# Kernel optimization log

Measured on AMD Instinct MI355X. Metric: run time of the kernel, lower is better.

The kernel has to match this reference:

```python
import jax, jax.numpy as jnp
import numpy as np

C0, C1 = 8, 4            # scalar / vector channels (type_in = type_out = [8,4])
K = 5                    # p-space kernel size
G = 8                    # number of gaussian radial basis functions
EPS = 1e-6               # zero-length epsilon
R_MAX = 5.5              # max |p_off - q_diff| ~ sqrt(3)*2 + 2


def _levi_civita():
    e = np.zeros((3, 3, 3), np.float32)
    e[0, 1, 2] = e[1, 2, 0] = e[2, 0, 1] = 1.0
    e[0, 2, 1] = e[2, 1, 0] = e[1, 0, 2] = -1.0
    return jnp.asarray(e)


def setup_inputs() -> dict:
    key = jax.random.key(0)
    ks = jax.random.split(key, 10)
    N, Q, P = 1, 16, 8
    dim = C0 + 3 * C1
    x = jax.random.normal(ks[0], (N, dim, Q, P, P, P), jnp.float32)

    def qschema(k):
        q = jax.random.normal(k, (Q, 3), jnp.float32)
        return q / jnp.max(jnp.linalg.norm(q, axis=-1))  # normalize lengths to <= 1

    q_in, q_out = qschema(ks[1]), qschema(ks[2])
    s = 0.1
    w_ss = s * jax.random.normal(ks[3], (C0, C0, G), jnp.float32)
    w_vs = s * jax.random.normal(ks[4], (C1, C0, G), jnp.float32)
    w_sv = s * jax.random.normal(ks[5], (C0, C1, G), jnp.float32)
    w_vv0 = s * jax.random.normal(ks[6], (C1, C1, G), jnp.float32)
    w_vv1 = s * jax.random.normal(ks[7], (C1, C1, G), jnp.float32)
    bias = s * jax.random.normal(ks[8], (C0,), jnp.float32)
    return dict(x=x, q_in=q_in, q_out=q_out, w_ss=w_ss, w_vs=w_vs, w_sv=w_sv,
                w_vv0=w_vv0, w_vv1=w_vv1, bias=bias)


def reference(x, q_in, q_out, w_ss, w_vs, w_sv, w_vv0, w_vv1, bias):
    N, dim_in, Qi = x.shape[0], x.shape[1], x.shape[2]
    Qo = q_out.shape[0]
    K3 = K ** 3
    # p-space tap offsets (voxel units, zyx) of the 5x5x5 kernel
    offs = jnp.arange(K, dtype=x.dtype) - (K - 1) / 2.0
    oz, oy, ox = jnp.meshgrid(offs, offs, offs, indexing='ij')
    p_off = jnp.stack([oz, oy, ox], -1).reshape(-1, 3)                       # (K3,3)
    # pq_diff geometry: v = p_offset - (q_out - q_in)
    v = p_off[None, None] - (q_out[:, None, None] - q_in[None, :, None])     # (Qo,Qi,K3,3)
    r = jnp.linalg.norm(v, axis=-1)                                          # (Qo,Qi,K3)
    u = jnp.where(r[..., None] > EPS, v / jnp.maximum(r, EPS)[..., None], 0.0)
    # gaussian radial basis on |v|
    centers = jnp.linspace(0.0, R_MAX, G).astype(x.dtype)
    sigma = R_MAX / (G - 1)
    R = jnp.exp(-0.5 * ((r[..., None] - centers) / sigma) ** 2)              # (Qo,Qi,K3,G)
    RY = R[..., None] * u[..., None, :]                                      # (Qo,Qi,K3,G,3) radial x Y_1
    eye3 = jnp.eye(3, dtype=x.dtype)
    eps3 = _levi_civita().astype(x.dtype)
    # CG paths (l_in,l_out,l_f): axes a=out ch, c=in ch, p=Qo, q=Qi, k=tap, g=radial, m/n/i/j=vec comps
    K_ss = jnp.einsum('acg,pqkg->apcqk', w_ss, R)                            # (0,0,0)
    K_vs = jnp.einsum('acg,pqkgm->ampcqk', w_vs, RY)                         # (0,1,1)
    K_sv = jnp.einsum('acg,pqkgm->apcmqk', w_sv, RY)                         # (1,0,1)
    K_vv = (jnp.einsum('acg,pqkg,mn->ampcnqk', w_vv0, R, eye3)               # (1,1,0) identity
            + 0.7071067811865476 *
            jnp.einsum('acg,pqkgm,imj->aipcjqk', w_vv1, RY, eps3))           # (1,1,1) cross prod
    top = jnp.concatenate([K_ss, K_sv.reshape(C0, Qo, 3 * C1, Qi, K3)], axis=2)
    bot = jnp.concatenate([K_vs.reshape(3 * C1, Qo, C0, Qi, K3),
                           K_vv.reshape(3 * C1, Qo, 3 * C1, Qi, K3)], axis=2)
    kern = jnp.concatenate([top, bot], axis=0)                               # (dim_out,Qo,dim_in,Qi,K3)
    dim_out = C0 + 3 * C1
    kern = kern.reshape(dim_out * Qo, dim_in * Qi, K, K, K)
    xr = x.reshape(N, dim_in * Qi, *x.shape[3:])
    out = jax.lax.conv_general_dilated(
        xr, kern, window_strides=(1, 1, 1), padding='SAME',
        dimension_numbers=('NCDHW', 'OIDHW', 'NCDHW'))
    out = out.reshape(N, dim_out, Qo, *x.shape[3:])
    b_full = jnp.concatenate([bias, jnp.zeros(3 * C1, bias.dtype)])
    return out + b_full.reshape(1, dim_out, 1, 1, 1, 1)
```

## Files before the change

kernel.cpp:

```cpp
#include <hip/hip_runtime.h>
#include <hip/hip_bf16.h>
#include <math.h>

#define C0 8
#define C1 4
#define NCH 20
#define NQ 16
#define K3 125
#define G 8
#define RMAX 5.5f
#define EPSL 1e-6f

#define KD1 2048
#define PHI_N 1048576
#define XTP_N 552960
#define W2_N 20480
#define E2C_B 10485760

#define LDS_A 16384
#define LDS_B 27648
#define LDS_SZ 44032

using f32x4 = __attribute__((ext_vector_type(4))) float;
using s16x8 = __attribute__((ext_vector_type(8))) short;

typedef const __attribute__((address_space(1))) unsigned int gq_t;
typedef __attribute__((address_space(3))) unsigned int lq_t;

__device__ __forceinline__ float epsf(int i, int m, int j) {
    if (i == m || m == j || i == j) return 0.f;
    return (m == (i + 1) % 3) ? 1.f : -1.f;
}

__global__ __launch_bounds__(256) void prep_kernel(
    const float* __restrict__ x,
    const float* __restrict__ q_in, const float* __restrict__ q_out,
    const float* __restrict__ w_ss, const float* __restrict__ w_vs,
    const float* __restrict__ w_sv, const float* __restrict__ w_vv0,
    const float* __restrict__ w_vv1,
    __hip_bfloat16* __restrict__ phi, __hip_bfloat16* __restrict__ xtp,
    __hip_bfloat16* __restrict__ w2)
{
    int gid = blockIdx.x * 256 + threadIdx.x;
    if (gid < PHI_N) {
        int col = gid & (KD1 - 1); int m = gid >> 11;
        int t = col >> 4, q = col & 15;
        int p = m >> 5,  b = m & 31;
        int g = b >> 2,  mi = b & 3;
        float val = 0.f;
        if (t < K3) {
            int tz = t / 25, ty = (t / 5) % 5, tx = t % 5;
            float vz = (float)(tz - 2) - (q_out[p*3+0] - q_in[q*3+0]);
            float vy = (float)(ty - 2) - (q_out[p*3+1] - q_in[q*3+1]);
            float vx = (float)(tx - 2) - (q_out[p*3+2] - q_in[q*3+2]);
            float r  = sqrtf(vz*vz + vy*vy + vx*vx);
            float inv = (r > EPSL) ? (1.0f / r) : 0.0f;
            const float sigma = RMAX / (float)(G - 1);
            float d = (r - (RMAX * (float)g / (float)(G - 1))) / sigma;
            float Rg = expf(-0.5f * d * d);
            float u = (mi == 1) ? vz*inv : ((mi == 2) ? vy*inv : vx*inv);
            val = (mi == 0) ? Rg : Rg * u;
        }
        phi[gid] = __float2bfloat16(val);
    } else if (gid < PHI_N + XTP_N) {
        int g2 = gid - PHI_N;
        int q = g2 & 15; int r = g2 >> 4;
        int ax = r % 12; r /= 12;
        int ay = r % 12; r /= 12;
        int az = r % 12; int c = r / 12;
        int iz = az - 2, iy = ay - 2, ix = ax - 2;
        bool valid = ((unsigned)iz < 8u) & ((unsigned)iy < 8u) & ((unsigned)ix < 8u);
        float v = valid ? x[((c * NQ + q) << 9) + (iz << 6) + (iy << 3) + ix] : 0.f;
        xtp[g2] = __float2bfloat16(v);
    } else {
        int id = gid - (PHI_N + XTP_N);
        int b = id & 31; int r = id >> 5;
        int c = r % NCH; int o = r / NCH;
        int g = b >> 2,  mi = b & 3;
        float val = 0.f;
        if (o < NCH) {
            if (o < C0) {
                if (c < C0) { if (mi == 0) val = w_ss[(o * C0 + c) * G + g]; }
                else { int cv = (c - C0) / 3, j = (c - C0) % 3;
                       if (mi == 1 + j) val = w_sv[(o * C1 + cv) * G + g]; }
            } else {
                int ov = (o - C0) / 3, i = (o - C0) % 3;
                if (c < C0) { if (mi == 1 + i) val = w_vs[(ov * C0 + c) * G + g]; }
                else {
                    int cv = (c - C0) / 3, j = (c - C0) % 3;
                    if (mi == 0) { if (i == j) val = w_vv0[(ov * C1 + cv) * G + g]; }
                    else val = 0.7071067811865476f * w_vv1[(ov * C1 + cv) * G + g]
                               * epsf(i, mi - 1, j);
                }
            }
        }
        w2[id] = __float2bfloat16(val);
    }
}

__global__ __launch_bounds__(256, 3) void gemm1_kernel(
    const char* __restrict__ phi_b, const char* __restrict__ xtp_b,
    char* __restrict__ E2_b)
{
    __shared__ __align__(16) char lds[LDS_SZ];

    int tid = threadIdx.x;
    int wave = tid >> 6, lane = tid & 63;
    int row = lane & 15, quad = lane >> 4;
    int wi = wave >> 1, wj = wave & 1;
    int hi = quad >> 1;

    int bi = blockIdx.x;
    int kc = bi / 320;
    int r  = bi - kc * 320;
    int pg = r / 80;
    int r2 = r - pg * 80;
    int c  = r2 >> 2;
    int zq = r2 & 3;

    {
        const char* src = xtp_b + c * 55296 + zq * 9216;
        for (int i = tid; i < 1728; i += 256) {
            int d = (i * 16) ^ (((i >> 1) & 7) << 4);
            *(s16x8*)(lds + LDS_A + d) = *(const s16x8*)(src + i * 16);
        }
    }

    const char* gA[4];
    {
        int lrow = lane >> 3;
        int cslot = (lane & 7) ^ (lrow & 7);
        #pragma unroll
        for (int i = 0; i < 4; ++i)
            gA[i] = phi_b + (size_t)(pg * 128 + wave * 32 + i * 8 + lrow) * 4096
                    + kc * 2048 + cslot * 16;
    }
    int arx = (row & 7) << 4;

    int bpre[4];
    #pragma unroll
    for (int nt = 0; nt < 4; ++nt) {
        int zl = wj * 64 + nt * 16 + row;
        int zz = zl >> 6, zy = (zl >> 3) & 7, zx = zl & 7;
        bpre[nt] = (zz * 144 + zy * 12 + zx) * 32 + (quad & 1) * 16;
    }

    f32x4 acc[4][4];
    #pragma unroll
    for (int i = 0; i < 4; ++i)
        #pragma unroll
        for (int j = 0; j < 4; ++j) acc[i][j] = (f32x4){0.f, 0.f, 0.f, 0.f};

    for (int j = 0; j < 16; ++j) {
        __syncthreads();
        #pragma unroll
        for (int i = 0; i < 4; ++i)
            __builtin_amdgcn_global_load_lds(
                (gq_t*)(gA[i] + j * 128),
                (lq_t*)(lds + (wave * 4 + i) * 1024), 16, 0, 0);
        __syncthreads();

        int toff[4];
        #pragma unroll
        for (int tt = 0; tt < 4; ++tt) {
            int t = kc * 64 + j * 4 + tt; if (t > 124) t = 124;
            int tz = t / 25, trm = t - tz * 25;
            int ty = trm / 5, tx = trm - ty * 5;
            toff[tt] = (tz * 144 + ty * 12 + tx) * 32;
        }
        #pragma unroll
        for (int st = 0; st < 2; ++st) {
            s16x8 af[4], bf[4];
            #pragma unroll
            for (int mt = 0; mt < 4; ++mt) {
                int aa = ((wi * 64 + mt * 16 + row) * 128 + (st * 4 + quad) * 16) ^ arx;
                af[mt] = *(const s16x8*)(lds + aa);
            }
            int tsel = toff[st * 2 + hi];
            #pragma unroll
            for (int nt = 0; nt < 4; ++nt) {
                int ba = bpre[nt] + tsel;
                ba ^= ((ba >> 5) & 7) << 4;
                bf[nt] = *(const s16x8*)(lds + LDS_A + ba);
            }
            #pragma unroll
            for (int mt = 0; mt < 4; ++mt)
                #pragma unroll
                for (int nt = 0; nt < 4; ++nt)
                    acc[mt][nt] = __builtin_amdgcn_mfma_f32_16x16x32_bf16(
                        af[mt], bf[nt], acc[mt][nt], 0, 0, 0);
        }
    }
    __syncthreads();

    int wbase = wave * 8704;
    #pragma unroll
    for (int mt = 0; mt < 4; ++mt) {
        #pragma unroll
        for (int nt = 0; nt < 4; ++nt) {
            int zl = nt * 16 + row;
            union { unsigned long long u; __hip_bfloat16 h[4]; } pk;
            pk.h[0] = __float2bfloat16(acc[mt][nt][0]);
            pk.h[1] = __float2bfloat16(acc[mt][nt][1]);
            pk.h[2] = __float2bfloat16(acc[mt][nt][2]);
            pk.h[3] = __float2bfloat16(acc[mt][nt][3]);
            *(unsigned long long*)(lds + wbase + zl * 136 + (mt * 16 + quad * 4) * 2) = pk.u;
        }
    }
    char* Ek = E2_b + (size_t)kc * E2C_B;
    int pbase = pg * 4 + wi * 2;
    #pragma unroll
    for (int it = 0; it < 8; ++it) {
        int item = lane + it * 64;
        int piece = item & 3;
        int zl = (item >> 2) & 63;
        int h  = item >> 8;
        s16x8 v = *(const s16x8*)(lds + wbase + zl * 136 + h * 64 + piece * 16);
        int p = pbase + h;
        int z = zq * 128 + wj * 64 + zl;
        *(s16x8*)(Ek + ((size_t)((p * NCH + c) << 9) + z) * 64 + piece * 16) = v;
    }
}

__global__ __launch_bounds__(128) void gemm2_kernel(
    const char* __restrict__ w2_b, const char* __restrict__ E2_b,
    const float* __restrict__ bias, float* __restrict__ out)
{
    int tid = threadIdx.x;
    int wave = tid >> 6, lane = tid & 63;
    int row = lane & 15, quad = lane >> 4;
    int bi = blockIdx.x;
    int p  = bi >> 4;
    int zb = bi & 15;
    int z  = zb * 32 + wave * 16 + row;

    const char* bbase = E2_b + (size_t)p * 655360 + (size_t)z * 64 + quad * 16;

    f32x4 acc[2];
    acc[0] = (f32x4){0.f, 0.f, 0.f, 0.f};
    acc[1] = (f32x4){0.f, 0.f, 0.f, 0.f};

    #pragma unroll
    for (int kc = 0; kc < 2; ++kc) {
        #pragma unroll 5
        for (int cc = 0; cc < 20; ++cc) {
            s16x8 a0 = *(const s16x8*)(w2_b + (row)      * 1280 + cc * 64 + quad * 16);
            s16x8 a1 = *(const s16x8*)(w2_b + (16 + row) * 1280 + cc * 64 + quad * 16);
            s16x8 b  = *(const s16x8*)(bbase + (size_t)kc * E2C_B + (size_t)cc * 32768);
            acc[0] = __builtin_amdgcn_mfma_f32_16x16x32_bf16(a0, b, acc[0], 0, 0, 0);
            acc[1] = __builtin_amdgcn_mfma_f32_16x16x32_bf16(a1, b, acc[1], 0, 0, 0);
        }
    }

    #pragma unroll
    for (int mt = 0; mt < 2; ++mt)
        #pragma unroll
        for (int ri = 0; ri < 4; ++ri) {
            int o = mt * 16 + quad * 4 + ri;
            if (o < NCH) {
                float v = acc[mt][ri];
                if (o < C0) v += bias[o];
                out[((o * NQ + p) << 9) + z] = v;
            }
        }
}

extern "C" void kernel_launch(void* const* d_in, const int* in_sizes, int n_in,
                              void* d_out, int out_size, void* d_ws, size_t ws_size,
                              hipStream_t stream) {
    const float* x     = (const float*)d_in[0];
    const float* q_in  = (const float*)d_in[1];
    const float* q_out = (const float*)d_in[2];
    const float* w_ss  = (const float*)d_in[3];
    const float* w_vs  = (const float*)d_in[4];
    const float* w_sv  = (const float*)d_in[5];
    const float* w_vv0 = (const float*)d_in[6];
    const float* w_vv1 = (const float*)d_in[7];
    const float* bias  = (const float*)d_in[8];
    float* out = (float*)d_out;

    char* ws = (char*)d_ws;
    __hip_bfloat16* phi = (__hip_bfloat16*)(ws + 0);
    __hip_bfloat16* xtp = (__hip_bfloat16*)(ws + 2097152);
    __hip_bfloat16* w2  = (__hip_bfloat16*)(ws + 3203072);
    char*           E2  = (char*)(ws + 3244032);

    const int PREP_N = PHI_N + XTP_N + W2_N;
    hipLaunchKernelGGL(prep_kernel, dim3(PREP_N / 256), dim3(256), 0, stream,
                       x, q_in, q_out, w_ss, w_vs, w_sv, w_vv0, w_vv1,
                       phi, xtp, w2);
    hipLaunchKernelGGL(gemm1_kernel, dim3(640), dim3(256), 0, stream,
                       (const char*)phi, (const char*)xtp, E2);
    hipLaunchKernelGGL(gemm2_kernel, dim3(256), dim3(128), 0, stream,
                       (const char*)w2, (const char*)E2, bias, out);
}
```

Measured before the change: 115.4 us.

## Double-buffer phi tiles in gemm1 and split-K gemm2 across four waves

gemm1 now keeps two LDS buffers for the phi A-tiles and issues the async global-to-LDS loads for the next k-step while the current step runs its MFMAs. The point is to hide global load latency. LDS use grows and the occupancy hint drops from 3 to 2 blocks. gemm2 goes from 2 to 8 waves per block, splits the 40-step K loop four ways, and reduces the partial sums through shared memory, giving more parallelism for the memory-bound second GEMM at the cost of a barrier and an LDS reduction.

```diff
diff --git a/kernel.cpp b/kernel.cpp
--- a/kernel.cpp
+++ b/kernel.cpp
@@ -19,7 +19,7 @@
 
 #define LDS_A 16384
 #define LDS_B 27648
-#define LDS_SZ 44032
+#define LDS_SZ 60416
 
 using f32x4 = __attribute__((ext_vector_type(4))) float;
 using s16x8 = __attribute__((ext_vector_type(8))) short;
@@ -98,7 +98,7 @@
     }
 }
 
-__global__ __launch_bounds__(256, 3) void gemm1_kernel(
+__global__ __launch_bounds__(256, 2) void gemm1_kernel(
     const char* __restrict__ phi_b, const char* __restrict__ xtp_b,
     char* __restrict__ E2_b)
 {
@@ -122,7 +122,7 @@
         const char* src = xtp_b + c * 55296 + zq * 9216;
         for (int i = tid; i < 1728; i += 256) {
             int d = (i * 16) ^ (((i >> 1) & 7) << 4);
-            *(s16x8*)(lds + LDS_A + d) = *(const s16x8*)(src + i * 16);
+            *(s16x8*)(lds + 2 * LDS_A + d) = *(const s16x8*)(src + i * 16);
         }
     }
 
@@ -151,14 +151,34 @@
         #pragma unroll
         for (int j = 0; j < 4; ++j) acc[i][j] = (f32x4){0.f, 0.f, 0.f, 0.f};
 
+    #pragma unroll
+    for (int i = 0; i < 4; ++i)
+        __builtin_amdgcn_global_load_lds(
+            (gq_t*)(gA[i]), (lq_t*)(lds + (wave * 4 + i) * 1024), 16, 0, 0);
+    asm volatile("s_waitcnt vmcnt(0) lgkmcnt(0)" ::: "memory");
+    __builtin_amdgcn_sched_barrier(0);
+    __builtin_amdgcn_s_barrier();
+    __builtin_amdgcn_sched_barrier(0);
+
+    int cur = 0;
     for (int j = 0; j < 16; ++j) {
-        __syncthreads();
-        #pragma unroll
-        for (int i = 0; i < 4; ++i)
-            __builtin_amdgcn_global_load_lds(
-                (gq_t*)(gA[i] + j * 128),
-                (lq_t*)(lds + (wave * 4 + i) * 1024), 16, 0, 0);
-        __syncthreads();
+        asm volatile("s_waitcnt lgkmcnt(0)" ::: "memory");
+        __builtin_amdgcn_sched_barrier(0);
+        __builtin_amdgcn_s_barrier();
+        __builtin_amdgcn_sched_barrier(0);
+        if (j < 15) {
+            #pragma unroll
+            for (int i = 0; i < 4; ++i)
+                __builtin_amdgcn_global_load_lds(
+                    (gq_t*)(gA[i] + (j + 1) * 128),
+                    (lq_t*)(lds + (cur ^ 1) * LDS_A + (wave * 4 + i) * 1024), 16, 0, 0);
+            asm volatile("s_waitcnt vmcnt(4)" ::: "memory");
+        } else {
+            asm volatile("s_waitcnt vmcnt(0)" ::: "memory");
+        }
+        __builtin_amdgcn_sched_barrier(0);
+        __builtin_amdgcn_s_barrier();
+        __builtin_amdgcn_sched_barrier(0);
 
         int toff[4];
         #pragma unroll
@@ -174,14 +194,14 @@
             #pragma unroll
             for (int mt = 0; mt < 4; ++mt) {
                 int aa = ((wi * 64 + mt * 16 + row) * 128 + (st * 4 + quad) * 16) ^ arx;
-                af[mt] = *(const s16x8*)(lds + aa);
+                af[mt] = *(const s16x8*)(lds + cur * LDS_A + aa);
             }
             int tsel = toff[st * 2 + hi];
             #pragma unroll
             for (int nt = 0; nt < 4; ++nt) {
                 int ba = bpre[nt] + tsel;
                 ba ^= ((ba >> 5) & 7) << 4;
-                bf[nt] = *(const s16x8*)(lds + LDS_A + ba);
+                bf[nt] = *(const s16x8*)(lds + 2 * LDS_A + ba);
             }
             #pragma unroll
             for (int mt = 0; mt < 4; ++mt)
@@ -190,6 +210,7 @@
                     acc[mt][nt] = __builtin_amdgcn_mfma_f32_16x16x32_bf16(
                         af[mt], bf[nt], acc[mt][nt], 0, 0, 0);
         }
+        cur ^= 1;
     }
     __syncthreads();
 
@@ -222,47 +243,68 @@
     }
 }
 
-__global__ __launch_bounds__(128) void gemm2_kernel(
+__global__ __launch_bounds__(512) void gemm2_kernel(
     const char* __restrict__ w2_b, const char* __restrict__ E2_b,
     const float* __restrict__ bias, float* __restrict__ out)
 {
+    __shared__ float red[3][2][64][8];
+
     int tid = threadIdx.x;
     int wave = tid >> 6, lane = tid & 63;
     int row = lane & 15, quad = lane >> 4;
+    int zh = wave & 1, ks = wave >> 1;
     int bi = blockIdx.x;
     int p  = bi >> 4;
     int zb = bi & 15;
-    int z  = zb * 32 + wave * 16 + row;
-
-    const char* bbase = E2_b + (size_t)p * 655360 + (size_t)z * 64 + quad * 16;
+    int z  = zb * 32 + zh * 16 + row;
+
+    int kcq = ks >> 1;
+    int cb  = (ks & 1) * 10;
+    const char* bbase = E2_b + (size_t)kcq * E2C_B + (size_t)p * 655360
+                        + (size_t)z * 64 + quad * 16;
 
     f32x4 acc[2];
     acc[0] = (f32x4){0.f, 0.f, 0.f, 0.f};
     acc[1] = (f32x4){0.f, 0.f, 0.f, 0.f};
 
     #pragma unroll
-    for (int kc = 0; kc < 2; ++kc) {
-        #pragma unroll 5
-        for (int cc = 0; cc < 20; ++cc) {
-            s16x8 a0 = *(const s16x8*)(w2_b + (row)      * 1280 + cc * 64 + quad * 16);
-            s16x8 a1 = *(const s16x8*)(w2_b + (16 + row) * 1280 + cc * 64 + quad * 16);
-            s16x8 b  = *(const s16x8*)(bbase + (size_t)kc * E2C_B + (size_t)cc * 32768);
-            acc[0] = __builtin_amdgcn_mfma_f32_16x16x32_bf16(a0, b, acc[0], 0, 0, 0);
-            acc[1] = __builtin_amdgcn_mfma_f32_16x16x32_bf16(a1, b, acc[1], 0, 0, 0);
-        }
-    }
-
-    #pragma unroll
-    for (int mt = 0; mt < 2; ++mt)
-        #pragma unroll
-        for (int ri = 0; ri < 4; ++ri) {
-            int o = mt * 16 + quad * 4 + ri;
-            if (o < NCH) {
-                float v = acc[mt][ri];
-                if (o < C0) v += bias[o];
-                out[((o * NQ + p) << 9) + z] = v;
+    for (int ci = 0; ci < 10; ++ci) {
+        int cc = cb + ci;
+        s16x8 a0 = *(const s16x8*)(w2_b + (row)      * 1280 + cc * 64 + quad * 16);
+        s16x8 a1 = *(const s16x8*)(w2_b + (16 + row) * 1280 + cc * 64 + quad * 16);
+        s16x8 b  = *(const s16x8*)(bbase + (size_t)cc * 32768);
+        acc[0] = __builtin_amdgcn_mfma_f32_16x16x32_bf16(a0, b, acc[0], 0, 0, 0);
+        acc[1] = __builtin_amdgcn_mfma_f32_16x16x32_bf16(a1, b, acc[1], 0, 0, 0);
+    }
+
+    if (ks != 0) {
+        #pragma unroll
+        for (int mt = 0; mt < 2; ++mt)
+            #pragma unroll
+            for (int ri = 0; ri < 4; ++ri)
+                red[ks - 1][zh][lane][mt * 4 + ri] = acc[mt][ri];
+    }
+    __syncthreads();
+    if (ks == 0) {
+        #pragma unroll
+        for (int s = 0; s < 3; ++s)
+            #pragma unroll
+            for (int mt = 0; mt < 2; ++mt)
+                #pragma unroll
+                for (int ri = 0; ri < 4; ++ri)
+                    acc[mt][ri] += red[s][zh][lane][mt * 4 + ri];
+        #pragma unroll
+        for (int mt = 0; mt < 2; ++mt)
+            #pragma unroll
+            for (int ri = 0; ri < 4; ++ri) {
+                int o = mt * 16 + quad * 4 + ri;
+                if (o < NCH) {
+                    float v = acc[mt][ri];
+                    if (o < C0) v += bias[o];
+                    out[((o * NQ + p) << 9) + z] = v;
+                }
             }
-        }
+    }
 }
 
 extern "C" void kernel_launch(void* const* d_in, const int* in_sizes, int n_in,
@@ -291,6 +333,6 @@
                        phi, xtp, w2);
     hipLaunchKernelGGL(gemm1_kernel, dim3(640), dim3(256), 0, stream,
                        (const char*)phi, (const char*)xtp, E2);
-    hipLaunchKernelGGL(gemm2_kernel, dim3(256), dim3(128), 0, stream,
+    hipLaunchKernelGGL(gemm2_kernel, dim3(256), dim3(512), 0, stream,
                        (const char*)w2, (const char*)E2, bias, out);
 }
```

New measurement: 119.5 us. 1.04x slower.
